# Kernel optimization log

Hardware: AMD Instinct MI355X
Metric: run time of the kernel (lower is better)

The kernel has to match this reference:

```python
import jax, jax.numpy as jnp
import numpy as np

N_NODES = 100000
N_EDGES = 1600000
D_IN = 64
D_OUT = 64


def setup_inputs() -> dict:
    key = jax.random.key(0)
    k1, k2, k3, k4 = jax.random.split(key, 4)
    x = jax.random.normal(k1, (N_NODES, D_IN), dtype=jnp.float32)
    edge_index = jax.random.randint(k2, (2, N_EDGES), 0, N_NODES, dtype=jnp.int64)
    W = jax.random.normal(k3, (D_OUT, D_IN), dtype=jnp.float32) * (1.0 / np.sqrt(D_IN))
    b = jax.random.normal(k4, (D_OUT,), dtype=jnp.float32) * 0.01
    return {"x": x, "edge_index": edge_index, "W": W, "b": b}


def reference(x, edge_index, W, b):
    num_nodes = x.shape[0]
    row, col = edge_index[0], edge_index[1]
    # degree of each node as a destination (scatter_add of ones over row)
    deg = jax.ops.segment_sum(jnp.ones(row.shape[0], dtype=x.dtype), row,
                              num_segments=num_nodes)
    # deg^-0.5 with inf (deg==0) replaced by 0
    deg_inv_sqrt = jnp.where(deg > 0, jax.lax.rsqrt(jnp.maximum(deg, 1.0)) * jnp.where(deg > 0, 1.0, 0.0), 0.0)
    deg_inv_sqrt = jnp.where(deg > 0, deg ** -0.5, 0.0)
    # gather source features, scale by source norm, scatter-add to destinations
    weighted = x[col] * deg_inv_sqrt[col][:, None]          # [E, D_IN]
    agg = jax.ops.segment_sum(weighted, row, num_segments=num_nodes)  # [N, D_IN]
    agg = agg * deg_inv_sqrt[:, None]
    # linear + relu (torch Linear: y = agg @ W.T + b)
    return jax.nn.relu(agg @ W.T + b)
```

## Files before the change

kernel.cpp:

```cpp
#include <hip/hip_runtime.h>

#define N_NODES 100000
#define N_EDGES 1600000
#define D 64

#define CSHIFT 7
#define CNODES 128
#define NCB 782
#define CAPC 2560
#define COLBITS 17
#define COLMASK 0x1FFFF

#define CHUNK 4096
#define EPT 16
#define NCHUNKA 391

#define CCUR_OFF   0
#define CPAIRS_OFF 3200
#define RS_OFF     8010880
#define DG_OFF     8410880
#define Y_OFF      8810880

typedef float fvec4 __attribute__((ext_vector_type(4)));
typedef __attribute__((ext_vector_type(8))) short bf16x8;
typedef __attribute__((ext_vector_type(4))) float f32x4;

__device__ __forceinline__ float bf2f(unsigned short u) {
    return __uint_as_float(((unsigned)u) << 16);
}
__device__ __forceinline__ unsigned f2bf(float f) {
    unsigned bits = __float_as_uint(f);
    return (bits + 0x7FFFu + ((bits >> 16) & 1u)) >> 16;
}

__global__ __launch_bounds__(256) void scatA_kernel(const int* __restrict__ row,
                                                    const int* __restrict__ col,
                                                    int* __restrict__ ccur,
                                                    int* __restrict__ cpairs) {
    __shared__ int lcnt[NCB];
    int t = threadIdx.x;
    int base = blockIdx.x * CHUNK;
    for (int i = t; i < NCB; i += 256) lcnt[i] = 0;
    __syncthreads();
    int r[EPT], c[EPT], pos[EPT];
#pragma unroll
    for (int i = 0; i < EPT; ++i) {
        int e = base + i * 256 + t;
        if (e < N_EDGES) {
            r[i] = row[e];
            c[i] = col[e];
            pos[i] = atomicAdd(&lcnt[r[i] >> CSHIFT], 1);
        } else r[i] = -1;
    }
    __syncthreads();
    for (int i = t; i < NCB; i += 256) {
        int cc = lcnt[i];
        lcnt[i] = cc ? atomicAdd(&ccur[i], cc) : 0;
    }
    __syncthreads();
#pragma unroll
    for (int i = 0; i < EPT; ++i) {
        if (r[i] >= 0) {
            int cb = r[i] >> CSHIFT;
            int p = lcnt[cb] + pos[i];
            if (p < CAPC)
                cpairs[cb * CAPC + p] = ((r[i] & (CNODES - 1)) << COLBITS) | c[i];
        }
    }
}

__global__ __launch_bounds__(256) void scatB_kernel(const int* __restrict__ ccur,
                                                    int* __restrict__ cpairs,
                                                    int* __restrict__ rs,
                                                    int* __restrict__ dg) {
    __shared__ int epk[CAPC];
    __shared__ int hist[CNODES];
    __shared__ int sc[CNODES];
    __shared__ int cur[CNODES];
    int t = threadIdx.x;
    int cb = blockIdx.x;
    int cnt = ccur[cb]; if (cnt > CAPC) cnt = CAPC;
    int base = cb * CAPC;
    if (t < CNODES) hist[t] = 0;
    __syncthreads();
    for (int i = t; i < cnt; i += 256) {
        int p = cpairs[base + i];
        epk[i] = p;
        atomicAdd(&hist[p >> COLBITS], 1);
    }
    __syncthreads();
    if (t < CNODES) sc[t] = hist[t];
    __syncthreads();
    for (int off = 1; off < CNODES; off <<= 1) {
        int v = (t < CNODES && t >= off) ? sc[t - off] : 0;
        __syncthreads();
        if (t < CNODES) sc[t] += v;
        __syncthreads();
    }
    if (t < CNODES) {
        int ex = sc[t] - hist[t];
        cur[t] = ex;
        int n = (cb << CSHIFT) + t;
        if (n < N_NODES) { rs[n] = base + ex; dg[n] = hist[t]; }
    }
    __syncthreads();
    for (int i = t; i < cnt; i += 256) {
        int p = epk[i];
        int pos = atomicAdd(&cur[p >> COLBITS], 1);
        cpairs[base + pos] = p & COLMASK;
    }
}

__global__ __launch_bounds__(256) void xform_kernel(
        const float* __restrict__ x, const float* __restrict__ W,
        const int* __restrict__ dg, unsigned short* __restrict__ y) {
    int t = threadIdx.x;
    int wave = t >> 6, lane = t & 63;
    int n0w = blockIdx.x * 64 + wave * 16;
    if (n0w >= N_NODES) return;
    int lm = lane & 15;
    int g  = lane >> 4;

    bf16x8 ahi[2], alo[2];
    const float* xr = x + (size_t)(n0w + lm) * D + g * 8;
#pragma unroll
    for (int ks = 0; ks < 2; ++ks) {
        float4 fa = *(const float4*)(xr + ks * 32);
        float4 fb = *(const float4*)(xr + ks * 32 + 4);
        float f[8] = {fa.x, fa.y, fa.z, fa.w, fb.x, fb.y, fb.z, fb.w};
#pragma unroll
        for (int j = 0; j < 8; ++j) {
            unsigned hb = f2bf(f[j]);
            float r = f[j] - bf2f((unsigned short)hb);
            ahi[ks][j] = (short)hb;
            alo[ks][j] = (short)f2bf(r);
        }
    }
    float dvr[4];
#pragma unroll
    for (int r = 0; r < 4; ++r) {
        int d = dg[n0w + g * 4 + r];
        dvr[r] = (d > 0) ? rsqrtf((float)d) : 0.0f;
    }
#pragma unroll
    for (int jt = 0; jt < 4; ++jt) {
        const float* wr = W + (size_t)(jt * 16 + lm) * D + g * 8;
        bf16x8 whi[2], wlo[2];
#pragma unroll
        for (int ks = 0; ks < 2; ++ks) {
            float4 fa = *(const float4*)(wr + ks * 32);
            float4 fb = *(const float4*)(wr + ks * 32 + 4);
            float f[8] = {fa.x, fa.y, fa.z, fa.w, fb.x, fb.y, fb.z, fb.w};
#pragma unroll
            for (int j = 0; j < 8; ++j) {
                unsigned hb = f2bf(f[j]);
                float r = f[j] - bf2f((unsigned short)hb);
                whi[ks][j] = (short)hb;
                wlo[ks][j] = (short)f2bf(r);
            }
        }
        f32x4 acc = {0.0f, 0.0f, 0.0f, 0.0f};
#pragma unroll
        for (int ks = 0; ks < 2; ++ks) {
            acc = __builtin_amdgcn_mfma_f32_16x16x32_bf16(ahi[ks], whi[ks], acc, 0, 0, 0);
            acc = __builtin_amdgcn_mfma_f32_16x16x32_bf16(alo[ks], whi[ks], acc, 0, 0, 0);
            acc = __builtin_amdgcn_mfma_f32_16x16x32_bf16(ahi[ks], wlo[ks], acc, 0, 0, 0);
        }
#pragma unroll
        for (int r = 0; r < 4; ++r) {
            int n = n0w + g * 4 + r;
            y[(size_t)n * D + jt * 16 + lm] = (unsigned short)f2bf(acc[r] * dvr[r]);
        }
    }
}

__global__ __launch_bounds__(256) void mega_kernel(
        const int* __restrict__ cols, const int* __restrict__ rs,
        const int* __restrict__ dg, const unsigned short* __restrict__ y,
        const float* __restrict__ bias, float* __restrict__ out) {
    __shared__ int scol[CAPC];
    int t = threadIdx.x;
    int b = blockIdx.x;
    int n0 = b * 64;
    int nlast = n0 + 63; if (nlast >= N_NODES) nlast = N_NODES - 1;
    int base = rs[n0];
    int cnt = rs[nlast] + dg[nlast] - base;
    for (int i = t; i < cnt; i += 256) scol[i] = cols[base + i];
    __syncthreads();
    int wave = t >> 6, lane = t & 63;
    int g = lane >> 3, q = lane & 7;
    float bj[8];
    {
        float4 b0 = *(const float4*)(bias + q * 8);
        float4 b1 = *(const float4*)(bias + q * 8 + 4);
        bj[0] = b0.x; bj[1] = b0.y; bj[2] = b0.z; bj[3] = b0.w;
        bj[4] = b1.x; bj[5] = b1.y; bj[6] = b1.z; bj[7] = b1.w;
    }
#pragma unroll 1
    for (int i = 0; i < 16; ++i) {
        int n = n0 + wave * 16 + i;
        if (n >= N_NODES) break;
        int s = rs[n] - base;
        int d = dg[n];
        float a[8];
#pragma unroll
        for (int j = 0; j < 8; ++j) a[j] = 0.0f;
        for (int k = 0; k < d; k += 32) {
#pragma unroll
            for (int u = 0; u < 4; ++u) {
                int e = k + u * 8 + g;
                if (e < d) {
                    int c = scol[s + e];
                    uint4 v = *(const uint4*)(y + (size_t)c * D + q * 8);
                    a[0] += __uint_as_float(v.x << 16);
                    a[1] += __uint_as_float(v.x & 0xffff0000u);
                    a[2] += __uint_as_float(v.y << 16);
                    a[3] += __uint_as_float(v.y & 0xffff0000u);
                    a[4] += __uint_as_float(v.z << 16);
                    a[5] += __uint_as_float(v.z & 0xffff0000u);
                    a[6] += __uint_as_float(v.w << 16);
                    a[7] += __uint_as_float(v.w & 0xffff0000u);
                }
            }
        }
#pragma unroll
        for (int m = 8; m <= 32; m <<= 1) {
#pragma unroll
            for (int j = 0; j < 8; ++j)
                a[j] += __shfl_xor(a[j], m);
        }
        float dv = (d > 0) ? rsqrtf((float)d) : 0.0f;
        if (g < 2) {
            int o = g * 4;
            fvec4 r;
            r.x = fmaxf(fmaf(dv, a[o + 0], bj[o + 0]), 0.0f);
            r.y = fmaxf(fmaf(dv, a[o + 1], bj[o + 1]), 0.0f);
            r.z = fmaxf(fmaf(dv, a[o + 2], bj[o + 2]), 0.0f);
            r.w = fmaxf(fmaf(dv, a[o + 3], bj[o + 3]), 0.0f);
            __builtin_nontemporal_store(r, (fvec4*)(out + (size_t)n * D + q * 8 + o));
        }
    }
}

extern "C" void kernel_launch(void* const* d_in, const int* in_sizes, int n_in,
                              void* d_out, int out_size, void* d_ws, size_t ws_size,
                              hipStream_t stream) {
    const float* x    = (const float*)d_in[0];
    const int*   eidx = (const int*)d_in[1];
    const float* W    = (const float*)d_in[2];
    const float* b    = (const float*)d_in[3];
    float* out = (float*)d_out;
    char* ws = (char*)d_ws;

    const int* row = eidx;
    const int* col = eidx + N_EDGES;

    int* ccur   = (int*)(ws + CCUR_OFF);
    int* cpairs = (int*)(ws + CPAIRS_OFF);
    int* rs     = (int*)(ws + RS_OFF);
    int* dg     = (int*)(ws + DG_OFF);
    unsigned short* y = (unsigned short*)(ws + Y_OFF);

    hipMemsetAsync(ccur, 0, NCB * sizeof(int), stream);
    scatA_kernel<<<NCHUNKA, 256, 0, stream>>>(row, col, ccur, cpairs);
    scatB_kernel<<<NCB, 256, 0, stream>>>(ccur, cpairs, rs, dg);
    xform_kernel<<<(N_NODES + 63) / 64, 256, 0, stream>>>(x, W, dg, y);
    mega_kernel<<<(N_NODES + 63) / 64, 256, 0, stream>>>(cpairs, rs, dg, y, b, out);
}
```

Before: 185.3 us.

## Fuse transform with edge bucketing and restructure aggregation to node-per-group gather

The dense transform and the first edge-bucketing pass now run as one launch, with blocks split by index. This removes a kernel boundary and lets the two independent stages overlap. Because the transform no longer needs degrees, source normalization moves into the aggregation: a new dinv array is computed in the second bucketing pass and gathered per edge. The aggregation kernel now assigns one node per 8-lane group instead of looping over 16 nodes per wave, drops the LDS staging of column indices, and prefetches the next four column indices. The cost is an extra random 4-byte dinv load per edge and possible load imbalance across nodes with different degrees.

```diff
diff --git a/kernel.cpp b/kernel.cpp
--- a/kernel.cpp
+++ b/kernel.cpp
@@ -11,15 +11,17 @@
 #define COLBITS 17
 #define COLMASK 0x1FFFF
 
-#define CHUNK 4096
-#define EPT 16
-#define NCHUNKA 391
+#define CHUNKA 2048
+#define EPTA 8
+#define NCHA 782
+#define XBLKS 1563
 
 #define CCUR_OFF   0
 #define CPAIRS_OFF 3200
 #define RS_OFF     8010880
 #define DG_OFF     8410880
-#define Y_OFF      8810880
+#define DINV_OFF   8810880
+#define Y_OFF      9210880
 
 typedef float fvec4 __attribute__((ext_vector_type(4)));
 typedef __attribute__((ext_vector_type(8))) short bf16x8;
@@ -33,46 +35,101 @@
     return (bits + 0x7FFFu + ((bits >> 16) & 1u)) >> 16;
 }
 
-__global__ __launch_bounds__(256) void scatA_kernel(const int* __restrict__ row,
-                                                    const int* __restrict__ col,
-                                                    int* __restrict__ ccur,
-                                                    int* __restrict__ cpairs) {
+__global__ __launch_bounds__(256) void fat_kernel(
+        const float* __restrict__ x, const float* __restrict__ W,
+        const int* __restrict__ row, const int* __restrict__ col,
+        int* __restrict__ ccur, int* __restrict__ cpairs,
+        unsigned short* __restrict__ y) {
     __shared__ int lcnt[NCB];
     int t = threadIdx.x;
-    int base = blockIdx.x * CHUNK;
-    for (int i = t; i < NCB; i += 256) lcnt[i] = 0;
-    __syncthreads();
-    int r[EPT], c[EPT], pos[EPT];
-#pragma unroll
-    for (int i = 0; i < EPT; ++i) {
-        int e = base + i * 256 + t;
-        if (e < N_EDGES) {
-            r[i] = row[e];
-            c[i] = col[e];
-            pos[i] = atomicAdd(&lcnt[r[i] >> CSHIFT], 1);
-        } else r[i] = -1;
-    }
-    __syncthreads();
-    for (int i = t; i < NCB; i += 256) {
-        int cc = lcnt[i];
-        lcnt[i] = cc ? atomicAdd(&ccur[i], cc) : 0;
-    }
-    __syncthreads();
-#pragma unroll
-    for (int i = 0; i < EPT; ++i) {
-        if (r[i] >= 0) {
-            int cb = r[i] >> CSHIFT;
-            int p = lcnt[cb] + pos[i];
-            if (p < CAPC)
-                cpairs[cb * CAPC + p] = ((r[i] & (CNODES - 1)) << COLBITS) | c[i];
-        }
-    }
-}
-
-__global__ __launch_bounds__(256) void scatB_kernel(const int* __restrict__ ccur,
+    if (blockIdx.x < XBLKS) {
+        int wave = t >> 6, lane = t & 63;
+        int n0w = blockIdx.x * 64 + wave * 16;
+        if (n0w >= N_NODES) return;
+        int lm = lane & 15;
+        int g  = lane >> 4;
+        bf16x8 ahi[2], alo[2];
+        const float* xr = x + (size_t)(n0w + lm) * D + g * 8;
+#pragma unroll
+        for (int ks = 0; ks < 2; ++ks) {
+            float4 fa = *(const float4*)(xr + ks * 32);
+            float4 fb = *(const float4*)(xr + ks * 32 + 4);
+            float f[8] = {fa.x, fa.y, fa.z, fa.w, fb.x, fb.y, fb.z, fb.w};
+#pragma unroll
+            for (int j = 0; j < 8; ++j) {
+                unsigned hb = f2bf(f[j]);
+                float r = f[j] - bf2f((unsigned short)hb);
+                ahi[ks][j] = (short)hb;
+                alo[ks][j] = (short)f2bf(r);
+            }
+        }
+#pragma unroll
+        for (int jt = 0; jt < 4; ++jt) {
+            const float* wr = W + (size_t)(jt * 16 + lm) * D + g * 8;
+            bf16x8 whi[2], wlo[2];
+#pragma unroll
+            for (int ks = 0; ks < 2; ++ks) {
+                float4 fa = *(const float4*)(wr + ks * 32);
+                float4 fb = *(const float4*)(wr + ks * 32 + 4);
+                float f[8] = {fa.x, fa.y, fa.z, fa.w, fb.x, fb.y, fb.z, fb.w};
+#pragma unroll
+                for (int j = 0; j < 8; ++j) {
+                    unsigned hb = f2bf(f[j]);
+                    float r = f[j] - bf2f((unsigned short)hb);
+                    whi[ks][j] = (short)hb;
+                    wlo[ks][j] = (short)f2bf(r);
+                }
+            }
+            f32x4 acc = {0.0f, 0.0f, 0.0f, 0.0f};
+#pragma unroll
+            for (int ks = 0; ks < 2; ++ks) {
+                acc = __builtin_amdgcn_mfma_f32_16x16x32_bf16(ahi[ks], whi[ks], acc, 0, 0, 0);
+                acc = __builtin_amdgcn_mfma_f32_16x16x32_bf16(alo[ks], whi[ks], acc, 0, 0, 0);
+                acc = __builtin_amdgcn_mfma_f32_16x16x32_bf16(ahi[ks], wlo[ks], acc, 0, 0, 0);
+            }
+#pragma unroll
+            for (int r = 0; r < 4; ++r) {
+                int n = n0w + g * 4 + r;
+                y[(size_t)n * D + jt * 16 + lm] = (unsigned short)f2bf(acc[r]);
+            }
+        }
+    } else {
+        int base = (blockIdx.x - XBLKS) * CHUNKA;
+        for (int i = t; i < NCB; i += 256) lcnt[i] = 0;
+        __syncthreads();
+        int r[EPTA], c[EPTA], pos[EPTA];
+#pragma unroll
+        for (int i = 0; i < EPTA; ++i) {
+            int e = base + i * 256 + t;
+            if (e < N_EDGES) {
+                r[i] = row[e];
+                c[i] = col[e];
+                pos[i] = atomicAdd(&lcnt[r[i] >> CSHIFT], 1);
+            } else r[i] = -1;
+        }
+        __syncthreads();
+        for (int i = t; i < NCB; i += 256) {
+            int cc = lcnt[i];
+            lcnt[i] = cc ? atomicAdd(&ccur[i], cc) : 0;
+        }
+        __syncthreads();
+#pragma unroll
+        for (int i = 0; i < EPTA; ++i) {
+            if (r[i] >= 0) {
+                int cb = r[i] >> CSHIFT;
+                int p = lcnt[cb] + pos[i];
+                if (p < CAPC)
+                    cpairs[cb * CAPC + p] = ((r[i] & (CNODES - 1)) << COLBITS) | c[i];
+            }
+        }
+    }
+}
+
+__global__ __launch_bounds__(512) void scatB_kernel(const int* __restrict__ ccur,
                                                     int* __restrict__ cpairs,
                                                     int* __restrict__ rs,
-                                                    int* __restrict__ dg) {
+                                                    int* __restrict__ dg,
+                                                    float* __restrict__ dinv) {
     __shared__ int epk[CAPC];
     __shared__ int hist[CNODES];
     __shared__ int sc[CNODES];
@@ -83,7 +140,7 @@
     int base = cb * CAPC;
     if (t < CNODES) hist[t] = 0;
     __syncthreads();
-    for (int i = t; i < cnt; i += 256) {
+    for (int i = t; i < cnt; i += 512) {
         int p = cpairs[base + i];
         epk[i] = p;
         atomicAdd(&hist[p >> COLBITS], 1);
@@ -101,94 +158,30 @@
         int ex = sc[t] - hist[t];
         cur[t] = ex;
         int n = (cb << CSHIFT) + t;
-        if (n < N_NODES) { rs[n] = base + ex; dg[n] = hist[t]; }
-    }
-    __syncthreads();
-    for (int i = t; i < cnt; i += 256) {
+        if (n < N_NODES) {
+            rs[n] = base + ex;
+            dg[n] = hist[t];
+            dinv[n] = (hist[t] > 0) ? rsqrtf((float)hist[t]) : 0.0f;
+        }
+    }
+    __syncthreads();
+    for (int i = t; i < cnt; i += 512) {
         int p = epk[i];
         int pos = atomicAdd(&cur[p >> COLBITS], 1);
         cpairs[base + pos] = p & COLMASK;
     }
 }
 
-__global__ __launch_bounds__(256) void xform_kernel(
-        const float* __restrict__ x, const float* __restrict__ W,
-        const int* __restrict__ dg, unsigned short* __restrict__ y) {
+__global__ __launch_bounds__(256) void mega_kernel(
+        const int* __restrict__ cols, const int* __restrict__ rs,
+        const int* __restrict__ dg, const float* __restrict__ dinv,
+        const unsigned short* __restrict__ y,
+        const float* __restrict__ bias, float* __restrict__ out) {
     int t = threadIdx.x;
     int wave = t >> 6, lane = t & 63;
-    int n0w = blockIdx.x * 64 + wave * 16;
-    if (n0w >= N_NODES) return;
-    int lm = lane & 15;
-    int g  = lane >> 4;
-
-    bf16x8 ahi[2], alo[2];
-    const float* xr = x + (size_t)(n0w + lm) * D + g * 8;
-#pragma unroll
-    for (int ks = 0; ks < 2; ++ks) {
-        float4 fa = *(const float4*)(xr + ks * 32);
-        float4 fb = *(const float4*)(xr + ks * 32 + 4);
-        float f[8] = {fa.x, fa.y, fa.z, fa.w, fb.x, fb.y, fb.z, fb.w};
-#pragma unroll
-        for (int j = 0; j < 8; ++j) {
-            unsigned hb = f2bf(f[j]);
-            float r = f[j] - bf2f((unsigned short)hb);
-            ahi[ks][j] = (short)hb;
-            alo[ks][j] = (short)f2bf(r);
-        }
-    }
-    float dvr[4];
-#pragma unroll
-    for (int r = 0; r < 4; ++r) {
-        int d = dg[n0w + g * 4 + r];
-        dvr[r] = (d > 0) ? rsqrtf((float)d) : 0.0f;
-    }
-#pragma unroll
-    for (int jt = 0; jt < 4; ++jt) {
-        const float* wr = W + (size_t)(jt * 16 + lm) * D + g * 8;
-        bf16x8 whi[2], wlo[2];
-#pragma unroll
-        for (int ks = 0; ks < 2; ++ks) {
-            float4 fa = *(const float4*)(wr + ks * 32);
-            float4 fb = *(const float4*)(wr + ks * 32 + 4);
-            float f[8] = {fa.x, fa.y, fa.z, fa.w, fb.x, fb.y, fb.z, fb.w};
-#pragma unroll
-            for (int j = 0; j < 8; ++j) {
-                unsigned hb = f2bf(f[j]);
-                float r = f[j] - bf2f((unsigned short)hb);
-                whi[ks][j] = (short)hb;
-                wlo[ks][j] = (short)f2bf(r);
-            }
-        }
-        f32x4 acc = {0.0f, 0.0f, 0.0f, 0.0f};
-#pragma unroll
-        for (int ks = 0; ks < 2; ++ks) {
-            acc = __builtin_amdgcn_mfma_f32_16x16x32_bf16(ahi[ks], whi[ks], acc, 0, 0, 0);
-            acc = __builtin_amdgcn_mfma_f32_16x16x32_bf16(alo[ks], whi[ks], acc, 0, 0, 0);
-            acc = __builtin_amdgcn_mfma_f32_16x16x32_bf16(ahi[ks], wlo[ks], acc, 0, 0, 0);
-        }
-#pragma unroll
-        for (int r = 0; r < 4; ++r) {
-            int n = n0w + g * 4 + r;
-            y[(size_t)n * D + jt * 16 + lm] = (unsigned short)f2bf(acc[r] * dvr[r]);
-        }
-    }
-}
-
-__global__ __launch_bounds__(256) void mega_kernel(
-        const int* __restrict__ cols, const int* __restrict__ rs,
-        const int* __restrict__ dg, const unsigned short* __restrict__ y,
-        const float* __restrict__ bias, float* __restrict__ out) {
-    __shared__ int scol[CAPC];
-    int t = threadIdx.x;
-    int b = blockIdx.x;
-    int n0 = b * 64;
-    int nlast = n0 + 63; if (nlast >= N_NODES) nlast = N_NODES - 1;
-    int base = rs[n0];
-    int cnt = rs[nlast] + dg[nlast] - base;
-    for (int i = t; i < cnt; i += 256) scol[i] = cols[base + i];
-    __syncthreads();
-    int wave = t >> 6, lane = t & 63;
     int g = lane >> 3, q = lane & 7;
+    int n = blockIdx.x * 32 + wave * 8 + g;
+    int s = rs[n], d = dg[n];
     float bj[8];
     {
         float4 b0 = *(const float4*)(bias + q * 8);
@@ -196,50 +189,55 @@
         bj[0] = b0.x; bj[1] = b0.y; bj[2] = b0.z; bj[3] = b0.w;
         bj[4] = b1.x; bj[5] = b1.y; bj[6] = b1.z; bj[7] = b1.w;
     }
-#pragma unroll 1
-    for (int i = 0; i < 16; ++i) {
-        int n = n0 + wave * 16 + i;
-        if (n >= N_NODES) break;
-        int s = rs[n] - base;
-        int d = dg[n];
-        float a[8];
-#pragma unroll
-        for (int j = 0; j < 8; ++j) a[j] = 0.0f;
-        for (int k = 0; k < d; k += 32) {
-#pragma unroll
-            for (int u = 0; u < 4; ++u) {
-                int e = k + u * 8 + g;
-                if (e < d) {
-                    int c = scol[s + e];
-                    uint4 v = *(const uint4*)(y + (size_t)c * D + q * 8);
-                    a[0] += __uint_as_float(v.x << 16);
-                    a[1] += __uint_as_float(v.x & 0xffff0000u);
-                    a[2] += __uint_as_float(v.y << 16);
-                    a[3] += __uint_as_float(v.y & 0xffff0000u);
-                    a[4] += __uint_as_float(v.z << 16);
-                    a[5] += __uint_as_float(v.z & 0xffff0000u);
-                    a[6] += __uint_as_float(v.w << 16);
-                    a[7] += __uint_as_float(v.w & 0xffff0000u);
-                }
-            }
-        }
-#pragma unroll
-        for (int m = 8; m <= 32; m <<= 1) {
-#pragma unroll
-            for (int j = 0; j < 8; ++j)
-                a[j] += __shfl_xor(a[j], m);
-        }
-        float dv = (d > 0) ? rsqrtf((float)d) : 0.0f;
-        if (g < 2) {
-            int o = g * 4;
-            fvec4 r;
-            r.x = fmaxf(fmaf(dv, a[o + 0], bj[o + 0]), 0.0f);
-            r.y = fmaxf(fmaf(dv, a[o + 1], bj[o + 1]), 0.0f);
-            r.z = fmaxf(fmaf(dv, a[o + 2], bj[o + 2]), 0.0f);
-            r.w = fmaxf(fmaf(dv, a[o + 3], bj[o + 3]), 0.0f);
-            __builtin_nontemporal_store(r, (fvec4*)(out + (size_t)n * D + q * 8 + o));
-        }
-    }
+    float a[8];
+#pragma unroll
+    for (int j = 0; j < 8; ++j) a[j] = 0.0f;
+    int c4[4];
+#pragma unroll
+    for (int u = 0; u < 4; ++u) c4[u] = (u < d) ? cols[s + u] : 0;
+    for (int k = 0; k < d; k += 4) {
+        uint4 v[4];
+        float dvl[4];
+#pragma unroll
+        for (int u = 0; u < 4; ++u) {
+            if (k + u < d) {
+                int c = c4[u];
+                dvl[u] = dinv[c];
+                v[u] = *(const uint4*)(y + (size_t)c * D + q * 8);
+            }
+        }
+#pragma unroll
+        for (int u = 0; u < 4; ++u) {
+            int e2 = k + 4 + u;
+            c4[u] = (e2 < d) ? cols[s + e2] : 0;
+        }
+#pragma unroll
+        for (int u = 0; u < 4; ++u) {
+            if (k + u < d) {
+                float dvu = dvl[u];
+                a[0] = fmaf(dvu, __uint_as_float(v[u].x << 16),        a[0]);
+                a[1] = fmaf(dvu, __uint_as_float(v[u].x & 0xffff0000u), a[1]);
+                a[2] = fmaf(dvu, __uint_as_float(v[u].y << 16),        a[2]);
+                a[3] = fmaf(dvu, __uint_as_float(v[u].y & 0xffff0000u), a[3]);
+                a[4] = fmaf(dvu, __uint_as_float(v[u].z << 16),        a[4]);
+                a[5] = fmaf(dvu, __uint_as_float(v[u].z & 0xffff0000u), a[5]);
+                a[6] = fmaf(dvu, __uint_as_float(v[u].w << 16),        a[6]);
+                a[7] = fmaf(dvu, __uint_as_float(v[u].w & 0xffff0000u), a[7]);
+            }
+        }
+    }
+    float dvn = dinv[n];
+    fvec4 r0, r1;
+    r0.x = fmaxf(fmaf(dvn, a[0], bj[0]), 0.0f);
+    r0.y = fmaxf(fmaf(dvn, a[1], bj[1]), 0.0f);
+    r0.z = fmaxf(fmaf(dvn, a[2], bj[2]), 0.0f);
+    r0.w = fmaxf(fmaf(dvn, a[3], bj[3]), 0.0f);
+    r1.x = fmaxf(fmaf(dvn, a[4], bj[4]), 0.0f);
+    r1.y = fmaxf(fmaf(dvn, a[5], bj[5]), 0.0f);
+    r1.z = fmaxf(fmaf(dvn, a[6], bj[6]), 0.0f);
+    r1.w = fmaxf(fmaf(dvn, a[7], bj[7]), 0.0f);
+    __builtin_nontemporal_store(r0, (fvec4*)(out + (size_t)n * D + q * 8));
+    __builtin_nontemporal_store(r1, (fvec4*)(out + (size_t)n * D + q * 8 + 4));
 }
 
 extern "C" void kernel_launch(void* const* d_in, const int* in_sizes, int n_in,
@@ -259,11 +257,11 @@
     int* cpairs = (int*)(ws + CPAIRS_OFF);
     int* rs     = (int*)(ws + RS_OFF);
     int* dg     = (int*)(ws + DG_OFF);
+    float* dinv = (float*)(ws + DINV_OFF);
     unsigned short* y = (unsigned short*)(ws + Y_OFF);
 
     hipMemsetAsync(ccur, 0, NCB * sizeof(int), stream);
-    scatA_kernel<<<NCHUNKA, 256, 0, stream>>>(row, col, ccur, cpairs);
-    scatB_kernel<<<NCB, 256, 0, stream>>>(ccur, cpairs, rs, dg);
-    xform_kernel<<<(N_NODES + 63) / 64, 256, 0, stream>>>(x, W, dg, y);
-    mega_kernel<<<(N_NODES + 63) / 64, 256, 0, stream>>>(cpairs, rs, dg, y, b, out);
-}
+    fat_kernel<<<XBLKS + NCHA, 256, 0, stream>>>(x, W, row, col, ccur, cpairs, y);
+    scatB_kernel<<<NCB, 512, 0, stream>>>(ccur, cpairs, rs, dg, dinv);
+    mega_kernel<<<3125, 256, 0, stream>>>(cpairs, rs, dg, dinv, y, b, out);
+}
```

New measurement: 169.9 us. 1.09x faster.
